# Optimization experiments

Measured on AMD Instinct MI355X. Metric: run time of the kernel, lower is better.

The kernel has to match this reference:

```python
import jax, jax.numpy as jnp
import numpy as np

EMBED_DIM = 256
NUM_HEADS = 8
N_Q = 300    # num queries
HW = 4096    # flattened key/value tokens
B = 16       # batch


def _linear(x, W, b):
    # torch nn.Linear: y = x @ W^T + b ; W is [out, in]
    return jnp.einsum('lbc,dc->lbd', x, W) + b


def setup_inputs() -> dict:
    key = jax.random.key(0)
    ks = jax.random.split(key, 32)
    C = EMBED_DIM
    s = 1.0 / np.sqrt(C)
    inp = {
        'query': jax.random.normal(ks[0], (N_Q, B, C), jnp.float32),
        'key': jax.random.normal(ks[1], (HW, B, C), jnp.float32),
        'value': jax.random.normal(ks[2], (HW, B, C), jnp.float32),
        'query_pos': jax.random.normal(ks[3], (N_Q, B, C), jnp.float32),
        'key_pos': jax.random.normal(ks[4], (HW, B, C), jnp.float32),
        'query_sine_embed': jax.random.normal(ks[5], (N_Q, B, C), jnp.float32),
    }
    names = ['qc', 'qp', 'qs', 'kc', 'kp', 'v', 'o']
    for i, nm in enumerate(names):
        inp[f'W_{nm}'] = jax.random.uniform(ks[6 + 2 * i], (C, C), jnp.float32, -s, s)
        inp[f'b_{nm}'] = jax.random.uniform(ks[7 + 2 * i], (C,), jnp.float32, -s, s)
    return inp


def reference(query, key, value, query_pos, key_pos, query_sine_embed,
              W_qc, b_qc, W_qp, b_qp, W_qs, b_qs, W_kc, b_kc,
              W_kp, b_kp, W_v, b_v, W_o, b_o):
    H = NUM_HEADS
    N, Bc, C = query.shape
    L = key.shape[0]
    Dh = C // H
    identity = query

    query_content = _linear(query, W_qc, b_qc)          # [N,B,C]
    key_content = _linear(key, W_kc, b_kc)              # [L,B,C]
    v = _linear(value, W_v, b_v)                        # [L,B,C]
    kp = _linear(key_pos, W_kp, b_kp)                   # [L,B,C]
    # is_first_layer == True branch
    qp = _linear(query_pos, W_qp, b_qp)                 # [N,B,C]
    q = query_content + qp
    k = key_content + kp

    qs = _linear(query_sine_embed, W_qs, b_qs)          # [N,B,C]
    # concat content and positional halves per head -> head dim 2*Dh
    q = jnp.concatenate([q.reshape(N, Bc, H, Dh), qs.reshape(N, Bc, H, Dh)], axis=3)
    k = jnp.concatenate([k.reshape(L, Bc, H, Dh), kp.reshape(L, Bc, H, Dh)], axis=3)

    q = q.transpose(1, 2, 0, 3)                          # [B,H,N,2Dh]
    k = k.transpose(1, 2, 0, 3)                          # [B,H,L,2Dh]
    v = v.reshape(L, Bc, H, Dh).transpose(1, 2, 0, 3)    # [B,H,L,Dh]

    scale = (2 * Dh) ** (-0.5)
    attn = jnp.einsum('bhnd,bhld->bhnl', q * scale, k)   # [B,H,N,L]
    attn = jax.nn.softmax(attn, axis=-1)
    out = jnp.einsum('bhnl,bhld->bhnd', attn, v)         # [B,H,N,Dh]
    out = out.transpose(0, 2, 1, 3).reshape(Bc, N, C)    # [B,N,C]
    out = jnp.einsum('bnc,dc->bnd', out, W_o) + b_o
    out = out.transpose(1, 0, 2)                         # [N,B,C]
    return identity + out
```

## Files before the change

### kernel.cpp

```cpp
#include <hip/hip_runtime.h>
#include <cstdint>
#include <cstddef>


typedef float  f4  __attribute__((ext_vector_type(4)));
typedef __bf16 b8v __attribute__((ext_vector_type(8)));

#define MFMA_BF16(a, b, c) __builtin_amdgcn_mfma_f32_16x16x32_bf16((a), (b), (c), 0, 0, 0)

#define GLD_LDS16(gp, lp)                                             \
  __builtin_amdgcn_global_load_lds(                                   \
      (const __attribute__((address_space(1))) void*)(gp),            \
      (__attribute__((address_space(3))) void*)(lp), 16, 0, 0)

#define KPLANE ((size_t)128 * 4096 * 32)

__global__ __launch_bounds__(256) void convert_w(
    const float* __restrict__ W0, const float* __restrict__ W1,
    const float* __restrict__ W2, __bf16* __restrict__ Wbf)
{
  int i = blockIdx.x * 256 + threadIdx.x;
  int base = i * 4;
  int m = base >> 16;
  int off = base & 65535;
  const float* W = (m == 0) ? W0 : (m == 1) ? W1 : W2;
  float4 v = *(const float4*)(W + off);
  __bf16 o[4];
  o[0] = (__bf16)v.x; o[1] = (__bf16)v.y; o[2] = (__bf16)v.z; o[3] = (__bf16)v.w;
  *(uint2*)(Wbf + (size_t)m * 65536 + off) = *(uint2*)o;
}

__global__ __launch_bounds__(256, 2) void key_side_gemm(
    const float* __restrict__ key, const float* __restrict__ key_pos,
    const float* __restrict__ value, const __bf16* __restrict__ Wbf,
    const float* __restrict__ b_kc, const float* __restrict__ b_kp,
    const float* __restrict__ b_v,
    __bf16* __restrict__ K64, __bf16* __restrict__ V32)
{
  __shared__ char smem[65536];
  const int tid  = threadIdx.x;
  const int wave = tid >> 6, lane = tid & 63;
  const int lrow = lane & 15, quad = lane >> 4;
  const int p  = blockIdx.y;
  const int lc = blockIdx.x >> 4;
  const int batch = blockIdx.x & 15;
  const int l0 = lc * 128;
  const int rowbase = (wave & 1) * 64;
  const int colbase = (wave >> 1) * 128;

  const float* __restrict__ X = (p == 0) ? key : (p == 1) ? key_pos : value;
  const __bf16* __restrict__ Wb = Wbf + (size_t)p * 65536;
  const float* __restrict__ bias = (p == 0) ? b_kc : (p == 1) ? b_kp : b_v;

  auto stageW = [&](int buf, int kc) {
#pragma unroll
    for (int it = 0; it < 8; ++it) {
      int slot = it * 256 + tid;
      int wr = slot >> 3, gp = slot & 7;
      int g  = gp ^ (wr & 7);
      GLD_LDS16(Wb + (size_t)wr * 256 + kc + g * 8, smem + buf * 32768 + slot * 16);
    }
  };
  auto readB = [&](int buf, int ct, int kk4) -> b8v {
    int wr = colbase + ct * 16 + lrow;
    int g  = (kk4 + quad) ^ (wr & 7);
    return *(const b8v*)(smem + buf * 32768 + wr * 128 + g * 16);
  };
  auto loadA = [&](float4* x0, float4* x1, int kc) {
#pragma unroll
    for (int rt = 0; rt < 4; ++rt) {
      const float* xp = X + ((size_t)(l0 + rowbase + rt * 16 + lrow) * 16 + batch) * 256
                          + kc + quad * 8;
      x0[rt] = *(const float4*)xp;
      x1[rt] = *(const float4*)(xp + 4);
    }
  };
  auto mk = [&](float4 x0, float4 x1) -> b8v {
    b8v t;
    t[0] = (__bf16)x0.x; t[1] = (__bf16)x0.y; t[2] = (__bf16)x0.z; t[3] = (__bf16)x0.w;
    t[4] = (__bf16)x1.x; t[5] = (__bf16)x1.y; t[6] = (__bf16)x1.z; t[7] = (__bf16)x1.w;
    return t;
  };

  f4 acc[4][8];
#pragma unroll
  for (int i = 0; i < 4; ++i)
#pragma unroll
    for (int j = 0; j < 8; ++j) acc[i][j] = f4{0.f, 0.f, 0.f, 0.f};

  float4 c0[4], c1[4], d0[4], d1[4];
  loadA(c0, c1, 0);
  stageW(0, 0);
  __syncthreads();

  for (int s = 0; s < 4; ++s) {
    const int kc0 = s * 64, buf = s & 1;
    loadA(d0, d1, kc0 + 32);
    if (s < 3) stageW(buf ^ 1, kc0 + 64);

    b8v a[4];
#pragma unroll
    for (int rt = 0; rt < 4; ++rt) a[rt] = mk(c0[rt], c1[rt]);
#pragma unroll
    for (int ct = 0; ct < 8; ++ct) {
      b8v bfr = readB(buf, ct, 0);
#pragma unroll
      for (int rt = 0; rt < 4; ++rt) acc[rt][ct] = MFMA_BF16(a[rt], bfr, acc[rt][ct]);
    }

    if (s < 3) loadA(c0, c1, kc0 + 64);

#pragma unroll
    for (int rt = 0; rt < 4; ++rt) a[rt] = mk(d0[rt], d1[rt]);
#pragma unroll
    for (int ct = 0; ct < 8; ++ct) {
      b8v bfr = readB(buf, ct, 4);
#pragma unroll
      for (int rt = 0; rt < 4; ++rt) acc[rt][ct] = MFMA_BF16(a[rt], bfr, acc[rt][ct]);
    }
    __syncthreads();
  }

  __bf16* Os = (__bf16*)smem;
#pragma unroll
  for (int ct = 0; ct < 8; ++ct) {
    int col = colbase + ct * 16 + lrow;
    float bv = bias[col];
    int cg = col >> 3, cr = col & 7;
#pragma unroll
    for (int rt = 0; rt < 4; ++rt)
#pragma unroll
      for (int r = 0; r < 4; ++r) {
        int row = rowbase + rt * 16 + quad * 4 + r;
        int g = cg ^ ((row ^ (row >> 3)) & 7);
        Os[row * 256 + g * 8 + cr] = (__bf16)(acc[rt][ct][r] + bv);
      }
  }
  __syncthreads();
#pragma unroll
  for (int it = 0; it < 16; ++it) {
    int h   = it >> 1;
    int row = (it & 1) * 64 + (tid >> 2);
    int seg = tid & 3;
    int g = (h * 4 + seg) ^ ((row ^ (row >> 3)) & 7);
    uint4 v = *(const uint4*)(Os + row * 256 + g * 8);
    size_t rowidx = ((size_t)(batch * 8 + h) * 4096) + l0 + row;
    if (p == 2) *(uint4*)(V32 + rowidx * 32 + seg * 8) = v;
    else        *(uint4*)(K64 + (size_t)p * KPLANE + rowidx * 32 + seg * 8) = v;
  }
}

__global__ __launch_bounds__(256) void query_side_gemm(
    const float* __restrict__ query, const float* __restrict__ query_pos,
    const float* __restrict__ query_sine,
    const float* __restrict__ W_qc, const float* __restrict__ b_qc,
    const float* __restrict__ W_qp, const float* __restrict__ b_qp,
    const float* __restrict__ W_qs, const float* __restrict__ b_qs,
    __bf16* __restrict__ Q64)
{
  __shared__ __bf16 Ws[256][72];
  const int tid  = threadIdx.x;
  const int wave = tid >> 6, lane = tid & 63;
  const int lrow = lane & 15, quad = lane >> 4;
  const int r0 = blockIdx.x * 64;

  f4 acc[16];
#pragma unroll
  for (int i = 0; i < 16; ++i) acc[i] = f4{0.f, 0.f, 0.f, 0.f};

  for (int kc = 0; kc < 768; kc += 64) {
    const float* X; const float* W;
    if (kc < 256)      { X = query;      W = W_qc; }
    else if (kc < 512) { X = query_pos;  W = W_qp; }
    else               { X = query_sine; W = W_qs; }
    const int ko = kc & 255;
#pragma unroll
    for (int it = 0; it < 16; ++it) {
      int idx = it * 256 + tid;
      int row = idx >> 4, c4 = idx & 15;
      float4 w = *(const float4*)(W + (size_t)row * 256 + ko + c4 * 4);
      __bf16* dp = &Ws[row][c4 * 4];
      dp[0] = (__bf16)w.x; dp[1] = (__bf16)w.y; dp[2] = (__bf16)w.z; dp[3] = (__bf16)w.w;
    }
    __syncthreads();
#pragma unroll
    for (int kk = 0; kk < 64; kk += 32) {
      const float* xp = X + (size_t)(r0 + wave * 16 + lrow) * 256 + ko + kk + quad * 8;
      float4 x0 = *(const float4*)xp;
      float4 x1 = *(const float4*)(xp + 4);
      b8v a;
      a[0] = (__bf16)x0.x; a[1] = (__bf16)x0.y; a[2] = (__bf16)x0.z; a[3] = (__bf16)x0.w;
      a[4] = (__bf16)x1.x; a[5] = (__bf16)x1.y; a[6] = (__bf16)x1.z; a[7] = (__bf16)x1.w;
#pragma unroll
      for (int ct = 0; ct < 16; ++ct) {
        b8v bf = *(const b8v*)&Ws[ct * 16 + lrow][kk + quad * 8];
        acc[ct] = MFMA_BF16(a, bf, acc[ct]);
      }
    }
    __syncthreads();
    if (kc == 448) {
#pragma unroll
      for (int ct = 0; ct < 16; ++ct) {
        int col = ct * 16 + lrow;
        float bsum = b_qc[col] + b_qp[col];
        int h = col >> 5, d = col & 31;
#pragma unroll
        for (int r = 0; r < 4; ++r) {
          int row = r0 + wave * 16 + quad * 4 + r;
          int n = row >> 4, bb = row & 15;
          Q64[((size_t)(bb * 8 + h) * 320 + n) * 64 + d] = (__bf16)((acc[ct][r] + bsum) * 0.125f);
        }
      }
    }
  }
#pragma unroll
  for (int ct = 0; ct < 16; ++ct) {
    int col = ct * 16 + lrow;
    float bsum = b_qc[col] + b_qp[col] + b_qs[col];
    int h = col >> 5, d = col & 31;
#pragma unroll
    for (int r = 0; r < 4; ++r) {
      int row = r0 + wave * 16 + quad * 4 + r;
      int n = row >> 4, bb = row & 15;
      Q64[((size_t)(bb * 8 + h) * 320 + n) * 64 + 32 + d] = (__bf16)((acc[ct][r] + bsum) * 0.125f);
    }
  }
}

__global__ __launch_bounds__(256, 2) void attn_part(
    const __bf16* __restrict__ Q64, const __bf16* __restrict__ K64,
    const __bf16* __restrict__ V32,
    __bf16* __restrict__ Opart, float* __restrict__ Mpart, float* __restrict__ Lpart)
{
  __shared__ __bf16 Ks[128 * 64];
  __shared__ __bf16 Vt[32][136];
  __shared__ __bf16 Pt[4][16][136];
  const int tid  = threadIdx.x;
  const int wave = tid >> 6, lane = tid & 63;
  const int lrow = lane & 15, quad = lane >> 4;
  const int ls = blockIdx.x, bh = blockIdx.y;
  const int l0base = ls * 1024;

  const __bf16* Kb0 = K64 + (size_t)bh * 4096 * 32;
  const __bf16* Kb1 = Kb0 + KPLANE;
  const __bf16* Vb  = V32 + (size_t)bh * 4096 * 32;

  b8v qa0[5], qa1[5];
#pragma unroll
  for (int t = 0; t < 5; ++t) {
    const __bf16* Qb = Q64 + ((size_t)bh * 320 + wave * 80 + t * 16 + lrow) * 64;
    qa0[t] = *(const b8v*)(Qb + quad * 8);
    qa1[t] = *(const b8v*)(Qb + 32 + quad * 8);
  }

  const int vs = tid & 3, vrh = tid >> 2;

  auto loadKV = [&](uint4* kr, uint4* vv, int c) {
    int l0 = l0base + c * 128;
#pragma unroll
    for (int it = 0; it < 4; ++it) {
      int slot = it * 256 + tid, row = slot >> 3, gs = slot & 7;
      int g = gs ^ (row & 7);
      const __bf16* src = (g < 4)
          ? (Kb0 + (size_t)(l0 + row) * 32 + g * 8)
          : (Kb1 + (size_t)(l0 + row) * 32 + (g - 4) * 8);
      kr[it] = *(const uint4*)src;
    }
    vv[0] = *(const uint4*)(Vb + (size_t)(l0 + 2 * vrh) * 32 + vs * 8);
    vv[1] = *(const uint4*)(Vb + (size_t)(l0 + 2 * vrh + 1) * 32 + vs * 8);
  };
  auto stage = [&](const uint4* kr, const uint4* vv) {
#pragma unroll
    for (int it = 0; it < 4; ++it) {
      int slot = it * 256 + tid;
      *(uint4*)((char*)Ks + slot * 16) = kr[it];
    }
    __bf16 a[8], b[8];
    *(uint4*)a = vv[0]; *(uint4*)b = vv[1];
#pragma unroll
    for (int j = 0; j < 8; ++j) {
      __bf16 pr[2] = {a[j], b[j]};
      *(uint32_t*)&Vt[vs * 8 + j][2 * vrh] = *(const uint32_t*)pr;
    }
  };
  auto readKA = [&](int wr, int g) -> b8v {
    int gs = g ^ (wr & 7);
    return *(const b8v*)((const char*)Ks + wr * 128 + gs * 16);
  };

  float mst[5], lst[5];
  f4 oacc[5][2];
#pragma unroll
  for (int t = 0; t < 5; ++t) {
    mst[t] = -1e30f; lst[t] = 0.f;
    oacc[t][0] = f4{0.f, 0.f, 0.f, 0.f};
    oacc[t][1] = f4{0.f, 0.f, 0.f, 0.f};
  }

  auto compute = [&]() {
#pragma unroll
    for (int t = 0; t < 5; ++t) {
      f4 sc[8];
#pragma unroll
      for (int ct = 0; ct < 8; ++ct) {
        b8v ka0 = readKA(ct * 16 + lrow, quad);
        b8v ka1 = readKA(ct * 16 + lrow, 4 + quad);
        f4 z = f4{0.f, 0.f, 0.f, 0.f};
        z = MFMA_BF16(ka0, qa0[t], z);
        z = MFMA_BF16(ka1, qa1[t], z);
        sc[ct] = z;
      }
      float mx = sc[0][0];
#pragma unroll
      for (int ct = 0; ct < 8; ++ct)
#pragma unroll
        for (int r = 0; r < 4; ++r) mx = fmaxf(mx, sc[ct][r]);
      mx = fmaxf(mx, __shfl_xor(mx, 16));
      mx = fmaxf(mx, __shfl_xor(mx, 32));
      float mnew = fmaxf(mst[t], mx);
      float alpha = __expf(mst[t] - mnew);
      mst[t] = mnew;
      float rsum = 0.f;
#pragma unroll
      for (int ct = 0; ct < 8; ++ct)
#pragma unroll
        for (int r = 0; r < 4; ++r) {
          sc[ct][r] = __expf(sc[ct][r] - mnew);
          rsum += sc[ct][r];
        }
      rsum += __shfl_xor(rsum, 16);
      rsum += __shfl_xor(rsum, 32);
      lst[t] = lst[t] * alpha + rsum;
#pragma unroll
      for (int c2 = 0; c2 < 2; ++c2)
#pragma unroll
        for (int r = 0; r < 4; ++r) oacc[t][c2][r] *= alpha;

#pragma unroll
      for (int ct = 0; ct < 8; ++ct) {
        __bf16 p4[4];
#pragma unroll
        for (int r = 0; r < 4; ++r) p4[r] = (__bf16)sc[ct][r];
        *(uint2*)&Pt[wave][lrow][ct * 16 + quad * 4] = *(const uint2*)p4;
      }
#pragma unroll
      for (int kt = 0; kt < 4; ++kt) {
        b8v pb = *(const b8v*)&Pt[wave][lrow][kt * 32 + quad * 8];
#pragma unroll
        for (int c2 = 0; c2 < 2; ++c2) {
          b8v va = *(const b8v*)&Vt[c2 * 16 + lrow][kt * 32 + quad * 8];
          oacc[t][c2] = MFMA_BF16(va, pb, oacc[t][c2]);
        }
      }
    }
  };

  uint4 kA[4], vA[2], kB[4], vB[2];
  loadKV(kA, vA, 0);
  for (int c = 0; c < 8; c += 2) {
    __syncthreads();
    stage(kA, vA);
    loadKV(kB, vB, c + 1);
    __syncthreads();
    compute();
    __syncthreads();
    stage(kB, vB);
    if (c + 2 < 8) loadKV(kA, vA, c + 2);
    __syncthreads();
    compute();
  }

  const size_t pbase = ((size_t)bh * 4 + ls) * 320;
#pragma unroll
  for (int t = 0; t < 5; ++t) {
    int q = wave * 80 + t * 16 + lrow;
    float inv = 1.0f / lst[t];
#pragma unroll
    for (int c2 = 0; c2 < 2; ++c2) {
      __bf16 o4[4];
#pragma unroll
      for (int r = 0; r < 4; ++r) o4[r] = (__bf16)(oacc[t][c2][r] * inv);
      *(uint2*)&Opart[(pbase + q) * 32 + c2 * 16 + quad * 4] = *(const uint2*)o4;
    }
    if (quad == 0) {
      Mpart[pbase + q] = mst[t];
      Lpart[pbase + q] = lst[t];
    }
  }
}

__global__ __launch_bounds__(256) void attn_combine(
    const __bf16* __restrict__ Opart, const float* __restrict__ Mpart,
    const float* __restrict__ Lpart, __bf16* __restrict__ Obf)
{
  const int bh = blockIdx.y;
  const int idx = blockIdx.x * 256 + threadIdx.x;
  const int q = idx >> 5, d = idx & 31;
  if (q >= 300) return;
  const size_t rb = ((size_t)bh * 4) * 320 + q;
  float m0 = Mpart[rb], m1 = Mpart[rb + 320], m2 = Mpart[rb + 640], m3 = Mpart[rb + 960];
  float M = fmaxf(fmaxf(m0, m1), fmaxf(m2, m3));
  float w0 = Lpart[rb]       * __expf(m0 - M);
  float w1 = Lpart[rb + 320] * __expf(m1 - M);
  float w2 = Lpart[rb + 640] * __expf(m2 - M);
  float w3 = Lpart[rb + 960] * __expf(m3 - M);
  float S = w0 + w1 + w2 + w3;
  float o = w0 * (float)Opart[rb * 32 + d]
          + w1 * (float)Opart[(rb + 320) * 32 + d]
          + w2 * (float)Opart[(rb + 640) * 32 + d]
          + w3 * (float)Opart[(rb + 960) * 32 + d];
  int b = bh >> 3, h = bh & 7;
  Obf[((size_t)b * 300 + q) * 256 + h * 32 + d] = (__bf16)(o / S);
}

__global__ __launch_bounds__(256) void out_proj_gemm(
    const __bf16* __restrict__ Obf, const float* __restrict__ W_o,
    const float* __restrict__ b_o, const float* __restrict__ query,
    float* __restrict__ out)
{
  __shared__ __bf16 Ws[256][72];
  const int tid  = threadIdx.x;
  const int wave = tid >> 6, lane = tid & 63;
  const int lrow = lane & 15, quad = lane >> 4;
  const int r0 = blockIdx.x * 64;

  f4 acc[16];
#pragma unroll
  for (int i = 0; i < 16; ++i) acc[i] = f4{0.f, 0.f, 0.f, 0.f};

  for (int kc0 = 0; kc0 < 256; kc0 += 64) {
#pragma unroll
    for (int it = 0; it < 16; ++it) {
      int idx = it * 256 + tid;
      int row = idx >> 4, c4 = idx & 15;
      float4 w = *(const float4*)(W_o + (size_t)row * 256 + kc0 + c4 * 4);
      __bf16* dp = &Ws[row][c4 * 4];
      dp[0] = (__bf16)w.x; dp[1] = (__bf16)w.y; dp[2] = (__bf16)w.z; dp[3] = (__bf16)w.w;
    }
    __syncthreads();
#pragma unroll
    for (int kk = 0; kk < 64; kk += 32) {
      b8v a = *(const b8v*)(Obf + (size_t)(r0 + wave * 16 + lrow) * 256 + kc0 + kk + quad * 8);
#pragma unroll
      for (int ct = 0; ct < 16; ++ct) {
        b8v bf = *(const b8v*)&Ws[ct * 16 + lrow][kk + quad * 8];
        acc[ct] = MFMA_BF16(a, bf, acc[ct]);
      }
    }
    __syncthreads();
  }
#pragma unroll
  for (int ct = 0; ct < 16; ++ct) {
    int col = ct * 16 + lrow;
    float bo = b_o[col];
#pragma unroll
    for (int r = 0; r < 4; ++r) {
      int row = r0 + wave * 16 + quad * 4 + r;
      int bb = row / 300, n = row % 300;
      size_t oaddr = ((size_t)n * 16 + bb) * 256 + col;
      out[oaddr] = acc[ct][r] + bo + query[oaddr];
    }
  }
}

extern "C" void kernel_launch(void* const* d_in, const int* in_sizes, int n_in,
                              void* d_out, int out_size, void* d_ws, size_t ws_size,
                              hipStream_t stream) {
  (void)in_sizes; (void)n_in; (void)out_size; (void)ws_size;
  const float* query      = (const float*)d_in[0];
  const float* key        = (const float*)d_in[1];
  const float* value      = (const float*)d_in[2];
  const float* query_pos  = (const float*)d_in[3];
  const float* key_pos    = (const float*)d_in[4];
  const float* query_sine = (const float*)d_in[5];
  const float* W_qc = (const float*)d_in[6];  const float* b_qc = (const float*)d_in[7];
  const float* W_qp = (const float*)d_in[8];  const float* b_qp = (const float*)d_in[9];
  const float* W_qs = (const float*)d_in[10]; const float* b_qs = (const float*)d_in[11];
  const float* W_kc = (const float*)d_in[12]; const float* b_kc = (const float*)d_in[13];
  const float* W_kp = (const float*)d_in[14]; const float* b_kp = (const float*)d_in[15];
  const float* W_v  = (const float*)d_in[16]; const float* b_v  = (const float*)d_in[17];
  const float* W_o  = (const float*)d_in[18]; const float* b_o  = (const float*)d_in[19];
  float* out = (float*)d_out;

  char* ws = (char*)d_ws;
  constexpr size_t K64_BYTES = (size_t)128 * 4096 * 64 * 2;
  constexpr size_t V32_BYTES = (size_t)128 * 4096 * 32 * 2;
  constexpr size_t Q64_BYTES = (size_t)128 * 320 * 64 * 2;
  constexpr size_t OBF_BYTES = (size_t)16 * 300 * 256 * 2;
  constexpr size_t WBF_BYTES = (size_t)3 * 256 * 256 * 2;
  constexpr size_t OPART_BYTES = (size_t)128 * 4 * 320 * 32 * 2;
  constexpr size_t MPART_BYTES = (size_t)128 * 4 * 320 * 4;
  __bf16* K64 = (__bf16*)ws;
  __bf16* V32 = (__bf16*)(ws + K64_BYTES);
  __bf16* Q64 = (__bf16*)(ws + K64_BYTES + V32_BYTES);
  __bf16* Obf = (__bf16*)(ws + K64_BYTES + V32_BYTES + Q64_BYTES);
  __bf16* Wbf = (__bf16*)(ws + K64_BYTES + V32_BYTES + Q64_BYTES + OBF_BYTES);
  char*  pbase = ws + K64_BYTES + V32_BYTES + Q64_BYTES + OBF_BYTES + WBF_BYTES;
  __bf16* Opart = (__bf16*)pbase;
  float*  Mpart = (float*)(pbase + OPART_BYTES);
  float*  Lpart = (float*)(pbase + OPART_BYTES + MPART_BYTES);

  hipLaunchKernelGGL(convert_w, dim3(192), dim3(256), 0, stream,
                     W_kc, W_kp, W_v, Wbf);
  hipLaunchKernelGGL(key_side_gemm, dim3(512, 3), dim3(256), 0, stream,
                     key, key_pos, value, Wbf, b_kc, b_kp, b_v, K64, V32);
  hipLaunchKernelGGL(query_side_gemm, dim3(75), dim3(256), 0, stream,
                     query, query_pos, query_sine, W_qc, b_qc, W_qp, b_qp, W_qs, b_qs, Q64);
  hipLaunchKernelGGL(attn_part, dim3(4, 128), dim3(256), 0, stream,
                     Q64, K64, V32, Opart, Mpart, Lpart);
  hipLaunchKernelGGL(attn_combine, dim3(40, 128), dim3(256), 0, stream,
                     Opart, Mpart, Lpart, Obf);
  hipLaunchKernelGGL(out_proj_gemm, dim3(75), dim3(256), 0, stream,
                     Obf, W_o, b_o, query, out);
}
```

Baseline: 460.9 us.

## Fuse weight conversion into query GEMM and split attention into eight key chunks

Merges the bf16 weight conversion into the query-side GEMM launch as extra blocks, which removes one kernel launch. The attention split-K grows from 4 to 8 chunks of 512 keys each, giving 1024 blocks instead of 512, and launch bounds are raised to 3 blocks per CU. The combine kernel now merges 8 partials. This trades more grid parallelism and occupancy for twice the partial-output traffic, a larger combine step, and possible register pressure from the tighter launch bound.

```diff
diff --git a/kernel.cpp b/kernel.cpp
--- a/kernel.cpp
+++ b/kernel.cpp
@@ -14,21 +14,6 @@
       (__attribute__((address_space(3))) void*)(lp), 16, 0, 0)
 
 #define KPLANE ((size_t)128 * 4096 * 32)
-
-__global__ __launch_bounds__(256) void convert_w(
-    const float* __restrict__ W0, const float* __restrict__ W1,
-    const float* __restrict__ W2, __bf16* __restrict__ Wbf)
-{
-  int i = blockIdx.x * 256 + threadIdx.x;
-  int base = i * 4;
-  int m = base >> 16;
-  int off = base & 65535;
-  const float* W = (m == 0) ? W0 : (m == 1) ? W1 : W2;
-  float4 v = *(const float4*)(W + off);
-  __bf16 o[4];
-  o[0] = (__bf16)v.x; o[1] = (__bf16)v.y; o[2] = (__bf16)v.z; o[3] = (__bf16)v.w;
-  *(uint2*)(Wbf + (size_t)m * 65536 + off) = *(uint2*)o;
-}
 
 __global__ __launch_bounds__(256, 2) void key_side_gemm(
     const float* __restrict__ key, const float* __restrict__ key_pos,
@@ -150,15 +135,29 @@
   }
 }
 
-__global__ __launch_bounds__(256) void query_side_gemm(
+__global__ __launch_bounds__(256) void query_conv(
     const float* __restrict__ query, const float* __restrict__ query_pos,
     const float* __restrict__ query_sine,
     const float* __restrict__ W_qc, const float* __restrict__ b_qc,
     const float* __restrict__ W_qp, const float* __restrict__ b_qp,
     const float* __restrict__ W_qs, const float* __restrict__ b_qs,
-    __bf16* __restrict__ Q64)
+    __bf16* __restrict__ Q64,
+    const float* __restrict__ W_kc, const float* __restrict__ W_kp,
+    const float* __restrict__ W_v, __bf16* __restrict__ Wbf)
 {
   __shared__ __bf16 Ws[256][72];
+  if (blockIdx.x >= 75) {
+    int i = (blockIdx.x - 75) * 256 + threadIdx.x;
+    int base = i * 4;
+    int m = base >> 16;
+    int off = base & 65535;
+    const float* W = (m == 0) ? W_kc : (m == 1) ? W_kp : W_v;
+    float4 v = *(const float4*)(W + off);
+    __bf16 o[4];
+    o[0] = (__bf16)v.x; o[1] = (__bf16)v.y; o[2] = (__bf16)v.z; o[3] = (__bf16)v.w;
+    *(uint2*)(Wbf + (size_t)m * 65536 + off) = *(uint2*)o;
+    return;
+  }
   const int tid  = threadIdx.x;
   const int wave = tid >> 6, lane = tid & 63;
   const int lrow = lane & 15, quad = lane >> 4;
@@ -227,7 +226,7 @@
   }
 }
 
-__global__ __launch_bounds__(256, 2) void attn_part(
+__global__ __launch_bounds__(256, 3) void attn_part(
     const __bf16* __restrict__ Q64, const __bf16* __restrict__ K64,
     const __bf16* __restrict__ V32,
     __bf16* __restrict__ Opart, float* __restrict__ Mpart, float* __restrict__ Lpart)
@@ -239,7 +238,7 @@
   const int wave = tid >> 6, lane = tid & 63;
   const int lrow = lane & 15, quad = lane >> 4;
   const int ls = blockIdx.x, bh = blockIdx.y;
-  const int l0base = ls * 1024;
+  const int l0base = ls * 512;
 
   const __bf16* Kb0 = K64 + (size_t)bh * 4096 * 32;
   const __bf16* Kb1 = Kb0 + KPLANE;
@@ -357,7 +356,7 @@
 
   uint4 kA[4], vA[2], kB[4], vB[2];
   loadKV(kA, vA, 0);
-  for (int c = 0; c < 8; c += 2) {
+  for (int c = 0; c < 4; c += 2) {
     __syncthreads();
     stage(kA, vA);
     loadKV(kB, vB, c + 1);
@@ -365,12 +364,12 @@
     compute();
     __syncthreads();
     stage(kB, vB);
-    if (c + 2 < 8) loadKV(kA, vA, c + 2);
+    if (c + 2 < 4) loadKV(kA, vA, c + 2);
     __syncthreads();
     compute();
   }
 
-  const size_t pbase = ((size_t)bh * 4 + ls) * 320;
+  const size_t pbase = ((size_t)bh * 8 + ls) * 320;
 #pragma unroll
   for (int t = 0; t < 5; ++t) {
     int q = wave * 80 + t * 16 + lrow;
@@ -397,18 +396,20 @@
   const int idx = blockIdx.x * 256 + threadIdx.x;
   const int q = idx >> 5, d = idx & 31;
   if (q >= 300) return;
-  const size_t rb = ((size_t)bh * 4) * 320 + q;
-  float m0 = Mpart[rb], m1 = Mpart[rb + 320], m2 = Mpart[rb + 640], m3 = Mpart[rb + 960];
-  float M = fmaxf(fmaxf(m0, m1), fmaxf(m2, m3));
-  float w0 = Lpart[rb]       * __expf(m0 - M);
-  float w1 = Lpart[rb + 320] * __expf(m1 - M);
-  float w2 = Lpart[rb + 640] * __expf(m2 - M);
-  float w3 = Lpart[rb + 960] * __expf(m3 - M);
-  float S = w0 + w1 + w2 + w3;
-  float o = w0 * (float)Opart[rb * 32 + d]
-          + w1 * (float)Opart[(rb + 320) * 32 + d]
-          + w2 * (float)Opart[(rb + 640) * 32 + d]
-          + w3 * (float)Opart[(rb + 960) * 32 + d];
+  const size_t rb = (size_t)bh * 8 * 320 + q;
+  float m[8];
+#pragma unroll
+  for (int j = 0; j < 8; ++j) m[j] = Mpart[rb + j * 320];
+  float M = m[0];
+#pragma unroll
+  for (int j = 1; j < 8; ++j) M = fmaxf(M, m[j]);
+  float S = 0.f, o = 0.f;
+#pragma unroll
+  for (int j = 0; j < 8; ++j) {
+    float w = Lpart[rb + j * 320] * __expf(m[j] - M);
+    S += w;
+    o += w * (float)Opart[(rb + j * 320) * 32 + d];
+  }
   int b = bh >> 3, h = bh & 7;
   Obf[((size_t)b * 300 + q) * 256 + h * 32 + d] = (__bf16)(o / S);
 }
@@ -488,8 +489,8 @@
   constexpr size_t Q64_BYTES = (size_t)128 * 320 * 64 * 2;
   constexpr size_t OBF_BYTES = (size_t)16 * 300 * 256 * 2;
   constexpr size_t WBF_BYTES = (size_t)3 * 256 * 256 * 2;
-  constexpr size_t OPART_BYTES = (size_t)128 * 4 * 320 * 32 * 2;
-  constexpr size_t MPART_BYTES = (size_t)128 * 4 * 320 * 4;
+  constexpr size_t OPART_BYTES = (size_t)128 * 8 * 320 * 32 * 2;
+  constexpr size_t MPART_BYTES = (size_t)128 * 8 * 320 * 4;
   __bf16* K64 = (__bf16*)ws;
   __bf16* V32 = (__bf16*)(ws + K64_BYTES);
   __bf16* Q64 = (__bf16*)(ws + K64_BYTES + V32_BYTES);
@@ -500,13 +501,12 @@
   float*  Mpart = (float*)(pbase + OPART_BYTES);
   float*  Lpart = (float*)(pbase + OPART_BYTES + MPART_BYTES);
 
-  hipLaunchKernelGGL(convert_w, dim3(192), dim3(256), 0, stream,
+  hipLaunchKernelGGL(query_conv, dim3(267), dim3(256), 0, stream,
+                     query, query_pos, query_sine, W_qc, b_qc, W_qp, b_qp, W_qs, b_qs, Q64,
                      W_kc, W_kp, W_v, Wbf);
   hipLaunchKernelGGL(key_side_gemm, dim3(512, 3), dim3(256), 0, stream,
                      key, key_pos, value, Wbf, b_kc, b_kp, b_v, K64, V32);
-  hipLaunchKernelGGL(query_side_gemm, dim3(75), dim3(256), 0, stream,
-                     query, query_pos, query_sine, W_qc, b_qc, W_qp, b_qp, W_qs, b_qs, Q64);
-  hipLaunchKernelGGL(attn_part, dim3(4, 128), dim3(256), 0, stream,
+  hipLaunchKernelGGL(attn_part, dim3(8, 128), dim3(256), 0, stream,
                      Q64, K64, V32, Opart, Mpart, Lpart);
   hipLaunchKernelGGL(attn_combine, dim3(40, 128), dim3(256), 0, stream,
                      Opart, Mpart, Lpart, Obf);
```

After: 614.9 us. 1.33x slower.

## Double-buffer attention K/V via direct global-to-LDS loads; fuse weight conversion into query GEMM

Applied to the files above, without the earlier changes.

The attention kernel now keeps two LDS buffers for K and V. K tiles are fetched with global_load_lds straight into the next buffer, and only V still passes through registers for its transpose. The loop needs one barrier per chunk instead of four, so loads overlap compute with less register staging. Separately, the bf16 weight conversion is folded into the query-side GEMM launch as extra blocks, removing one kernel launch. Doubled LDS use may lower occupancy, and the single barrier relies on the async LDS write having completed before the next compute, which is not waited on explicitly.

```diff
diff --git a/kernel.cpp b/kernel.cpp
--- a/kernel.cpp
+++ b/kernel.cpp
@@ -14,21 +14,6 @@
       (__attribute__((address_space(3))) void*)(lp), 16, 0, 0)
 
 #define KPLANE ((size_t)128 * 4096 * 32)
-
-__global__ __launch_bounds__(256) void convert_w(
-    const float* __restrict__ W0, const float* __restrict__ W1,
-    const float* __restrict__ W2, __bf16* __restrict__ Wbf)
-{
-  int i = blockIdx.x * 256 + threadIdx.x;
-  int base = i * 4;
-  int m = base >> 16;
-  int off = base & 65535;
-  const float* W = (m == 0) ? W0 : (m == 1) ? W1 : W2;
-  float4 v = *(const float4*)(W + off);
-  __bf16 o[4];
-  o[0] = (__bf16)v.x; o[1] = (__bf16)v.y; o[2] = (__bf16)v.z; o[3] = (__bf16)v.w;
-  *(uint2*)(Wbf + (size_t)m * 65536 + off) = *(uint2*)o;
-}
 
 __global__ __launch_bounds__(256, 2) void key_side_gemm(
     const float* __restrict__ key, const float* __restrict__ key_pos,
@@ -150,15 +135,29 @@
   }
 }
 
-__global__ __launch_bounds__(256) void query_side_gemm(
+__global__ __launch_bounds__(256) void query_conv(
     const float* __restrict__ query, const float* __restrict__ query_pos,
     const float* __restrict__ query_sine,
     const float* __restrict__ W_qc, const float* __restrict__ b_qc,
     const float* __restrict__ W_qp, const float* __restrict__ b_qp,
     const float* __restrict__ W_qs, const float* __restrict__ b_qs,
-    __bf16* __restrict__ Q64)
+    __bf16* __restrict__ Q64,
+    const float* __restrict__ W_kc, const float* __restrict__ W_kp,
+    const float* __restrict__ W_v, __bf16* __restrict__ Wbf)
 {
   __shared__ __bf16 Ws[256][72];
+  if (blockIdx.x >= 75) {
+    int i = (blockIdx.x - 75) * 256 + threadIdx.x;
+    int base = i * 4;
+    int m = base >> 16;
+    int off = base & 65535;
+    const float* W = (m == 0) ? W_kc : (m == 1) ? W_kp : W_v;
+    float4 v = *(const float4*)(W + off);
+    __bf16 o[4];
+    o[0] = (__bf16)v.x; o[1] = (__bf16)v.y; o[2] = (__bf16)v.z; o[3] = (__bf16)v.w;
+    *(uint2*)(Wbf + (size_t)m * 65536 + off) = *(uint2*)o;
+    return;
+  }
   const int tid  = threadIdx.x;
   const int wave = tid >> 6, lane = tid & 63;
   const int lrow = lane & 15, quad = lane >> 4;
@@ -232,8 +231,8 @@
     const __bf16* __restrict__ V32,
     __bf16* __restrict__ Opart, float* __restrict__ Mpart, float* __restrict__ Lpart)
 {
-  __shared__ __bf16 Ks[128 * 64];
-  __shared__ __bf16 Vt[32][136];
+  __shared__ __bf16 Ks[2][128 * 64];
+  __shared__ __bf16 Vt[2][32][136];
   __shared__ __bf16 Pt[4][16][136];
   const int tid  = threadIdx.x;
   const int wave = tid >> 6, lane = tid & 63;
@@ -255,7 +254,7 @@
 
   const int vs = tid & 3, vrh = tid >> 2;
 
-  auto loadKV = [&](uint4* kr, uint4* vv, int c) {
+  auto issueK = [&](int buf, int c) {
     int l0 = l0base + c * 128;
 #pragma unroll
     for (int it = 0; it < 4; ++it) {
@@ -264,28 +263,26 @@
       const __bf16* src = (g < 4)
           ? (Kb0 + (size_t)(l0 + row) * 32 + g * 8)
           : (Kb1 + (size_t)(l0 + row) * 32 + (g - 4) * 8);
-      kr[it] = *(const uint4*)src;
-    }
+      GLD_LDS16(src, (char*)&Ks[buf][0] + slot * 16);
+    }
+  };
+  auto loadV = [&](uint4* vv, int c) {
+    int l0 = l0base + c * 128;
     vv[0] = *(const uint4*)(Vb + (size_t)(l0 + 2 * vrh) * 32 + vs * 8);
     vv[1] = *(const uint4*)(Vb + (size_t)(l0 + 2 * vrh + 1) * 32 + vs * 8);
   };
-  auto stage = [&](const uint4* kr, const uint4* vv) {
-#pragma unroll
-    for (int it = 0; it < 4; ++it) {
-      int slot = it * 256 + tid;
-      *(uint4*)((char*)Ks + slot * 16) = kr[it];
-    }
+  auto stageV = [&](int buf, const uint4* vv) {
     __bf16 a[8], b[8];
     *(uint4*)a = vv[0]; *(uint4*)b = vv[1];
 #pragma unroll
     for (int j = 0; j < 8; ++j) {
       __bf16 pr[2] = {a[j], b[j]};
-      *(uint32_t*)&Vt[vs * 8 + j][2 * vrh] = *(const uint32_t*)pr;
-    }
-  };
-  auto readKA = [&](int wr, int g) -> b8v {
+      *(uint32_t*)&Vt[buf][vs * 8 + j][2 * vrh] = *(const uint32_t*)pr;
+    }
+  };
+  auto readKA = [&](int buf, int wr, int g) -> b8v {
     int gs = g ^ (wr & 7);
-    return *(const b8v*)((const char*)Ks + wr * 128 + gs * 16);
+    return *(const b8v*)((const char*)&Ks[buf][0] + wr * 128 + gs * 16);
   };
 
   float mst[5], lst[5];
@@ -297,14 +294,14 @@
     oacc[t][1] = f4{0.f, 0.f, 0.f, 0.f};
   }
 
-  auto compute = [&]() {
+  auto compute = [&](int buf) {
 #pragma unroll
     for (int t = 0; t < 5; ++t) {
       f4 sc[8];
 #pragma unroll
       for (int ct = 0; ct < 8; ++ct) {
-        b8v ka0 = readKA(ct * 16 + lrow, quad);
-        b8v ka1 = readKA(ct * 16 + lrow, 4 + quad);
+        b8v ka0 = readKA(buf, ct * 16 + lrow, quad);
+        b8v ka1 = readKA(buf, ct * 16 + lrow, 4 + quad);
         f4 z = f4{0.f, 0.f, 0.f, 0.f};
         z = MFMA_BF16(ka0, qa0[t], z);
         z = MFMA_BF16(ka1, qa1[t], z);
@@ -348,26 +345,25 @@
         b8v pb = *(const b8v*)&Pt[wave][lrow][kt * 32 + quad * 8];
 #pragma unroll
         for (int c2 = 0; c2 < 2; ++c2) {
-          b8v va = *(const b8v*)&Vt[c2 * 16 + lrow][kt * 32 + quad * 8];
+          b8v va = *(const b8v*)&Vt[buf][c2 * 16 + lrow][kt * 32 + quad * 8];
           oacc[t][c2] = MFMA_BF16(va, pb, oacc[t][c2]);
         }
       }
     }
   };
 
-  uint4 kA[4], vA[2], kB[4], vB[2];
-  loadKV(kA, vA, 0);
-  for (int c = 0; c < 8; c += 2) {
+  uint4 vv[2];
+  issueK(0, 0);
+  loadV(vv, 0);
+  for (int c = 0; c < 8; ++c) {
+    const int cur = c & 1;
+    stageV(cur, vv);
     __syncthreads();
-    stage(kA, vA);
-    loadKV(kB, vB, c + 1);
-    __syncthreads();
-    compute();
-    __syncthreads();
-    stage(kB, vB);
-    if (c + 2 < 8) loadKV(kA, vA, c + 2);
-    __syncthreads();
-    compute();
+    if (c + 1 < 8) {
+      issueK(cur ^ 1, c + 1);
+      loadV(vv, c + 1);
+    }
+    compute(cur);
   }
 
   const size_t pbase = ((size_t)bh * 4 + ls) * 320;
@@ -500,12 +496,11 @@
   float*  Mpart = (float*)(pbase + OPART_BYTES);
   float*  Lpart = (float*)(pbase + OPART_BYTES + MPART_BYTES);
 
-  hipLaunchKernelGGL(convert_w, dim3(192), dim3(256), 0, stream,
+  hipLaunchKernelGGL(query_conv, dim3(267), dim3(256), 0, stream,
+                     query, query_pos, query_sine, W_qc, b_qc, W_qp, b_qp, W_qs, b_qs, Q64,
                      W_kc, W_kp, W_v, Wbf);
   hipLaunchKernelGGL(key_side_gemm, dim3(512, 3), dim3(256), 0, stream,
                      key, key_pos, value, Wbf, b_kc, b_kp, b_v, K64, V32);
-  hipLaunchKernelGGL(query_side_gemm, dim3(75), dim3(256), 0, stream,
-                     query, query_pos, query_sine, W_qc, b_qc, W_qp, b_qp, W_qs, b_qs, Q64);
   hipLaunchKernelGGL(attn_part, dim3(4, 128), dim3(256), 0, stream,
                      Q64, K64, V32, Opart, Mpart, Lpart);
   hipLaunchKernelGGL(attn_combine, dim3(40, 128), dim3(256), 0, stream,
```

Result: faster. 401.1 us (-13.0%).
